# Optimization experiments

Measured on AMD Instinct MI355X. Metric: run time of the kernel, lower is better.

## Reference

```python
import jax, jax.numpy as jnp
import numpy as np

N = 500000
D = 128
R = D // 4  # reduction = 4
G = 2048    # number of graphs


def setup_inputs() -> dict:
    key = jax.random.key(0)
    ks = jax.random.split(key, 8)
    x = jax.random.normal(ks[0], (N, D), dtype=jnp.float32)
    batch = jnp.sort(jax.random.randint(ks[1], (N,), 0, G))
    # SE-gate MLP params (nn.Linear stores weight as [out,in]; we store transposed for x @ W)
    fc_w1 = jax.random.normal(ks[2], (D, R), dtype=jnp.float32) * (1.0 / np.sqrt(D))
    fc_b1 = jnp.zeros((R,), dtype=jnp.float32)
    fc_w2 = jax.random.normal(ks[3], (R, D), dtype=jnp.float32) * (1.0 / np.sqrt(R))
    fc_b2 = jnp.zeros((D,), dtype=jnp.float32)
    # xavier-uniform weight_matrix [D, D]
    lim = np.sqrt(6.0 / (D + D))
    W = jax.random.uniform(ks[4], (D, D), dtype=jnp.float32, minval=-lim, maxval=lim)
    return {"x": x, "batch": batch, "size": G,
            "fc_w1": fc_w1, "fc_b1": fc_b1, "fc_w2": fc_w2, "fc_b2": fc_b2, "W": W}


def reference(x, batch, size, fc_w1, fc_b1, fc_w2, fc_b2, W):
    # gated SE-block: attention = tanh(MLP(x)); x = attention*x + x
    attention = jnp.tanh(jnp.maximum(x @ fc_w1 + fc_b1, 0.0) @ fc_w2 + fc_b2)
    x2 = attention * x + x  # [N, D]
    # global_mean_pool: segment mean over graphs
    seg_sum = jax.ops.segment_sum(x2, batch, num_segments=size)           # [G, D]
    counts = jax.ops.segment_sum(jnp.ones((x2.shape[0],), x2.dtype), batch, num_segments=size)
    mean = seg_sum / jnp.maximum(counts, 1.0)[:, None]                     # [G, D]
    transformed_global = jnp.tanh(mean @ W)                                # [G, D]
    # gather-broadcast per-graph global back to nodes, per-node attention coef
    coefs = jax.nn.sigmoid(jnp.sum(x2 * transformed_global[batch], axis=1))  # [N]
    weighted = coefs[:, None] * x2                                          # [N, D]
    return jax.ops.segment_sum(weighted, batch, num_segments=size)          # [G, D]
```

## Files before the change

kernel.cpp:

```cpp
#include <hip/hip_runtime.h>
#include <hip/hip_bf16.h>

#define DDIM 128
#define RDIM 32
#define PBLK 256
#define BLK  512
#define CAP  160
#define XS2  136
#define HSTR 40

typedef __attribute__((ext_vector_type(8))) short bf16x8;
typedef __attribute__((ext_vector_type(4))) float f32x4;

__device__ __forceinline__ float tanh_fast(float v) {
  float e = __expf(2.f * v);
  return 1.f - 2.f / (e + 1.f);
}
__device__ __forceinline__ float sigmoid_fast(float v) {
  return 1.f / (1.f + __expf(-v));
}
__device__ __forceinline__ unsigned short f2bf(float f) {
  unsigned u = __float_as_uint(f);
  u += 0x7fffu + ((u >> 16) & 1u);
  return (unsigned short)(u >> 16);
}
__device__ __forceinline__ float bf2f(unsigned short s) {
  return __uint_as_float(((unsigned)s) << 16);
}
__device__ __forceinline__ unsigned pkbf(float lo, float hi) {
  __hip_bfloat162 t2 = __float22bfloat162_rn(make_float2(lo, hi));
  return *reinterpret_cast<unsigned*>(&t2);
}
__device__ __forceinline__ int lower_bound(const int* __restrict__ b, int n, int v) {
  int lo = 0, hi = n;
  while (lo < hi) { int m = (lo + hi) >> 1; if (b[m] < v) lo = m + 1; else hi = m; }
  return lo;
}

__global__ void k0_prep(const float* __restrict__ w1, const float* __restrict__ w2,
                        unsigned short* __restrict__ w1tf, unsigned short* __restrict__ w2tf)
{
  const int i  = blockIdx.x * blockDim.x + threadIdx.x;
  const int l  = i & 63;
  const int lr = l & 15, q = l >> 4;
  if (i < 512) {
    const int frag = i >> 6;
    const int mt2 = frag >> 2, kk = frag & 3;
    bf16x8 v;
    #pragma unroll
    for (int j = 0; j < 8; ++j)
      v[j] = (short)f2bf(w1[(size_t)(kk * 32 + q * 8 + j) * RDIM + mt2 * 16 + lr]);
    *(bf16x8*)&w1tf[(size_t)i * 8] = v;
  } else {
    const int mt = (i - 512) >> 6;
    bf16x8 v;
    #pragma unroll
    for (int j = 0; j < 8; ++j)
      v[j] = (short)f2bf(w2[(size_t)(q * 8 + j) * DDIM + mt * 16 + lr]);
    *(bf16x8*)&w2tf[(size_t)(i - 512) * 8] = v;
  }
}

__global__ void kb_bounds(const int* __restrict__ batch, int* __restrict__ bounds,
                          int N, int G)
{
  const int g = blockIdx.x * blockDim.x + threadIdx.x;
  if (g <= G) bounds[g] = lower_bound(batch, N, g);
}

__global__ __launch_bounds__(BLK, 4) void k_fused(
    const float* __restrict__ x,
    const unsigned short* __restrict__ w1tf, const float* __restrict__ b1,
    const unsigned short* __restrict__ w2tf, const float* __restrict__ b2,
    const float* __restrict__ W, const int* __restrict__ bounds,
    float* __restrict__ out, int N)
{
  __shared__ unsigned short w1t[512 * 8];
  __shared__ unsigned short w2t[512 * 8];
  __shared__ unsigned short x2s[CAP * XS2];
  __shared__ unsigned short hs8[8][16 * HSTR];
  __shared__ float part[8][132];
  __shared__ float meanv[DDIM];
  __shared__ float tgs[DDIM];

  const int t  = threadIdx.x;
  const int l  = t & 63;
  const int w  = t >> 6;
  const int lr = l & 15;
  const int q  = l >> 4;
  const int g  = blockIdx.x;
  const int lo = bounds[g], hi = bounds[g + 1];
  const int cnt = hi - lo;
  unsigned short* hs = hs8[w];

  for (int i = t; i < 512; i += BLK) {
    ((bf16x8*)w1t)[i] = ((const bf16x8*)w1tf)[i];
    ((bf16x8*)w2t)[i] = ((const bf16x8*)w2tf)[i];
  }
  __syncthreads();

  auto core = [&](int tb, f32x4 (&cacc)[8]) -> const float* {
    const int ridx = tb + lr;
    const int rcl  = min(ridx, cnt - 1);
    const float* xrow = x + (size_t)(lo + rcl) * DDIM;
    bf16x8 xf[4];
    #pragma unroll
    for (int kk = 0; kk < 4; ++kk) {
      float4 a = *(const float4*)(xrow + kk * 32 + q * 8);
      float4 b = *(const float4*)(xrow + kk * 32 + q * 8 + 4);
      uint4 u;
      u.x = pkbf(a.x, a.y); u.y = pkbf(a.z, a.w);
      u.z = pkbf(b.x, b.y); u.w = pkbf(b.z, b.w);
      xf[kk] = *(bf16x8*)&u;
    }
    f32x4 hacc[2];
    {
      float4 bv0 = *(const float4*)(b1 + q * 4);
      float4 bv1 = *(const float4*)(b1 + 16 + q * 4);
      hacc[0][0] = bv0.x; hacc[0][1] = bv0.y; hacc[0][2] = bv0.z; hacc[0][3] = bv0.w;
      hacc[1][0] = bv1.x; hacc[1][1] = bv1.y; hacc[1][2] = bv1.z; hacc[1][3] = bv1.w;
    }
    #pragma unroll
    for (int kk = 0; kk < 4; ++kk) {
      bf16x8 wa = *(const bf16x8*)&w1t[(size_t)((0 * 4 + kk) * 64 + l) * 8];
      bf16x8 wb = *(const bf16x8*)&w1t[(size_t)((1 * 4 + kk) * 64 + l) * 8];
      hacc[0] = __builtin_amdgcn_mfma_f32_16x16x32_bf16(wa, xf[kk], hacc[0], 0, 0, 0);
      hacc[1] = __builtin_amdgcn_mfma_f32_16x16x32_bf16(wb, xf[kk], hacc[1], 0, 0, 0);
    }
    #pragma unroll
    for (int mt2 = 0; mt2 < 2; ++mt2) {
      float h0 = fmaxf(hacc[mt2][0], 0.f), h1 = fmaxf(hacc[mt2][1], 0.f);
      float h2 = fmaxf(hacc[mt2][2], 0.f), h3 = fmaxf(hacc[mt2][3], 0.f);
      uint2 p; p.x = pkbf(h0, h1); p.y = pkbf(h2, h3);
      *(uint2*)&hs[lr * HSTR + mt2 * 16 + q * 4] = p;
    }
    bf16x8 ah = *(const bf16x8*)&hs[lr * HSTR + q * 8];
    #pragma unroll
    for (int mt = 0; mt < 8; ++mt) {
      float4 bv = *(const float4*)(b2 + mt * 16 + q * 4);
      cacc[mt][0] = bv.x; cacc[mt][1] = bv.y; cacc[mt][2] = bv.z; cacc[mt][3] = bv.w;
    }
    #pragma unroll
    for (int mt = 0; mt < 8; ++mt) {
      bf16x8 wf = *(const bf16x8*)&w2t[(size_t)(mt * 64 + l) * 8];
      cacc[mt] = __builtin_amdgcn_mfma_f32_16x16x32_bf16(wf, ah, cacc[mt], 0, 0, 0);
    }
    return xrow;
  };

  float macc[8][4];
  #pragma unroll
  for (int mt = 0; mt < 8; ++mt)
    #pragma unroll
    for (int c = 0; c < 4; ++c) macc[mt][c] = 0.f;

  const int niter1 = (cnt + 127) >> 7;
  for (int it = 0; it < niter1; ++it) {
    const int tb = it * 128 + w * 16;
    if (tb >= cnt) continue;
    f32x4 cacc[8];
    const float* xrow = core(tb, cacc);
    const int ridx = tb + lr;
    if (ridx < cnt) {
      #pragma unroll
      for (int mt = 0; mt < 8; ++mt) {
        float4 xg = *(const float4*)(xrow + mt * 16 + q * 4);
        float y0 = xg.x * (1.f + tanh_fast(cacc[mt][0]));
        float y1 = xg.y * (1.f + tanh_fast(cacc[mt][1]));
        float y2 = xg.z * (1.f + tanh_fast(cacc[mt][2]));
        float y3 = xg.w * (1.f + tanh_fast(cacc[mt][3]));
        macc[mt][0] += y0; macc[mt][1] += y1;
        macc[mt][2] += y2; macc[mt][3] += y3;
        if (ridx < CAP) {
          uint2 p; p.x = pkbf(y0, y1); p.y = pkbf(y2, y3);
          *(uint2*)&x2s[ridx * XS2 + mt * 16 + q * 4] = p;
        }
      }
    }
  }
  __syncthreads();

  #pragma unroll
  for (int mt = 0; mt < 8; ++mt)
    #pragma unroll
    for (int c = 0; c < 4; ++c) {
      float v = macc[mt][c];
      v += __shfl_xor(v, 1, 64);
      v += __shfl_xor(v, 2, 64);
      v += __shfl_xor(v, 4, 64);
      v += __shfl_xor(v, 8, 64);
      macc[mt][c] = v;
    }
  if (lr == 0) {
    #pragma unroll
    for (int mt = 0; mt < 8; ++mt)
      *(float4*)&part[w][mt * 16 + q * 4] =
          make_float4(macc[mt][0], macc[mt][1], macc[mt][2], macc[mt][3]);
  }
  __syncthreads();
  if (t < DDIM) {
    float m = 0.f;
    #pragma unroll
    for (int w2 = 0; w2 < 8; ++w2) m += part[w2][t];
    meanv[t] = (cnt > 0) ? m / (float)cnt : 0.f;
  }
  __syncthreads();

  {
    const int c = t & 127, s = t >> 7;
    float a = 0.f;
    #pragma unroll
    for (int k = 0; k < 32; ++k)
      a = fmaf(meanv[s * 32 + k], W[(size_t)(s * 32 + k) * DDIM + c], a);
    part[s][c] = a;
  }
  __syncthreads();
  if (t < DDIM)
    tgs[t] = tanh_fast(part[0][t] + part[1][t] + part[2][t] + part[3][t]);
  __syncthreads();

  float oacc[8][4];
  #pragma unroll
  for (int mt = 0; mt < 8; ++mt)
    #pragma unroll
    for (int c = 0; c < 4; ++c) oacc[mt][c] = 0.f;

  const int cap2 = cnt < CAP ? cnt : CAP;
  const int niter2 = (cap2 + 127) >> 7;
  for (int it = 0; it < niter2; ++it) {
    const int tb = it * 128 + w * 16;
    if (tb >= cap2) continue;
    const int ridx = tb + lr;
    const bool v = ridx < cap2;
    const int rr = v ? ridx : 0;
    float xv[8][4];
    float p = 0.f;
    #pragma unroll
    for (int mt = 0; mt < 8; ++mt) {
      uint2 u = *(const uint2*)&x2s[rr * XS2 + mt * 16 + q * 4];
      xv[mt][0] = bf2f((unsigned short)(u.x & 0xffffu));
      xv[mt][1] = bf2f((unsigned short)(u.x >> 16));
      xv[mt][2] = bf2f((unsigned short)(u.y & 0xffffu));
      xv[mt][3] = bf2f((unsigned short)(u.y >> 16));
      float4 tg4 = *(const float4*)&tgs[mt * 16 + q * 4];
      p = fmaf(xv[mt][0], tg4.x, p); p = fmaf(xv[mt][1], tg4.y, p);
      p = fmaf(xv[mt][2], tg4.z, p); p = fmaf(xv[mt][3], tg4.w, p);
    }
    p += __shfl_xor(p, 16, 64);
    p += __shfl_xor(p, 32, 64);
    const float coef = sigmoid_fast(p);
    if (v) {
      #pragma unroll
      for (int mt = 0; mt < 8; ++mt)
        #pragma unroll
        for (int c = 0; c < 4; ++c) oacc[mt][c] = fmaf(coef, xv[mt][c], oacc[mt][c]);
    }
  }

  if (cnt > CAP) {
    const int niter3 = (cnt - CAP + 127) >> 7;
    for (int it = 0; it < niter3; ++it) {
      const int tb = CAP + it * 128 + w * 16;
      if (tb >= cnt) continue;
      f32x4 cacc[8];
      const float* xrow = core(tb, cacc);
      const int ridx = tb + lr;
      const bool v = ridx < cnt;
      float p = 0.f;
      uint2 y2[8];
      #pragma unroll
      for (int mt = 0; mt < 8; ++mt) {
        float4 xg = *(const float4*)(xrow + mt * 16 + q * 4);
        float y0 = xg.x * (1.f + tanh_fast(cacc[mt][0]));
        float y1 = xg.y * (1.f + tanh_fast(cacc[mt][1]));
        float y2v = xg.z * (1.f + tanh_fast(cacc[mt][2]));
        float y3 = xg.w * (1.f + tanh_fast(cacc[mt][3]));
        float4 tg4 = *(const float4*)&tgs[mt * 16 + q * 4];
        p = fmaf(y0, tg4.x, p); p = fmaf(y1, tg4.y, p);
        p = fmaf(y2v, tg4.z, p); p = fmaf(y3, tg4.w, p);
        y2[mt].x = pkbf(y0, y1); y2[mt].y = pkbf(y2v, y3);
      }
      p += __shfl_xor(p, 16, 64);
      p += __shfl_xor(p, 32, 64);
      const float coef = sigmoid_fast(p);
      if (v) {
        #pragma unroll
        for (int mt = 0; mt < 8; ++mt) {
          oacc[mt][0] = fmaf(coef, bf2f((unsigned short)(y2[mt].x & 0xffffu)), oacc[mt][0]);
          oacc[mt][1] = fmaf(coef, bf2f((unsigned short)(y2[mt].x >> 16)),     oacc[mt][1]);
          oacc[mt][2] = fmaf(coef, bf2f((unsigned short)(y2[mt].y & 0xffffu)), oacc[mt][2]);
          oacc[mt][3] = fmaf(coef, bf2f((unsigned short)(y2[mt].y >> 16)),     oacc[mt][3]);
        }
      }
    }
  }
  __syncthreads();

  #pragma unroll
  for (int mt = 0; mt < 8; ++mt)
    #pragma unroll
    for (int c = 0; c < 4; ++c) {
      float v = oacc[mt][c];
      v += __shfl_xor(v, 1, 64);
      v += __shfl_xor(v, 2, 64);
      v += __shfl_xor(v, 4, 64);
      v += __shfl_xor(v, 8, 64);
      oacc[mt][c] = v;
    }
  if (lr == 0) {
    #pragma unroll
    for (int mt = 0; mt < 8; ++mt)
      *(float4*)&part[w][mt * 16 + q * 4] =
          make_float4(oacc[mt][0], oacc[mt][1], oacc[mt][2], oacc[mt][3]);
  }
  __syncthreads();
  if (t < DDIM) {
    float m = 0.f;
    #pragma unroll
    for (int w2 = 0; w2 < 8; ++w2) m += part[w2][t];
    out[(size_t)g * DDIM + t] = m;
  }
}

extern "C" void kernel_launch(void* const* d_in, const int* in_sizes, int n_in,
                              void* d_out, int out_size, void* d_ws, size_t ws_size,
                              hipStream_t stream) {
  const float* x     = (const float*)d_in[0];
  const int*   batch = (const int*)d_in[1];
  const float* w1 = (const float*)d_in[3];
  const float* b1 = (const float*)d_in[4];
  const float* w2 = (const float*)d_in[5];
  const float* b2 = (const float*)d_in[6];
  const float* W  = (const float*)d_in[7];
  float* out = (float*)d_out;

  const int N = in_sizes[0] / DDIM;
  const int G = out_size / DDIM;

  unsigned short* w1tf = (unsigned short*)d_ws;
  unsigned short* w2tf = w1tf + 4096;
  int* bounds = (int*)(w2tf + 4096);
  (void)ws_size; (void)n_in;

  hipLaunchKernelGGL(k0_prep, dim3(4), dim3(PBLK), 0, stream, w1, w2, w1tf, w2tf);
  hipLaunchKernelGGL(kb_bounds, dim3((G + 1 + PBLK - 1) / PBLK), dim3(PBLK), 0, stream,
                     batch, bounds, N, G);
  hipLaunchKernelGGL(k_fused, dim3(G), dim3(BLK), 0, stream,
                     x, w1tf, b1, w2tf, b2, W, bounds, out, N);
}
```

Measured before the change: 156.5 us.

## Halve block size and double-buffer x row loads across iterations

```diff
diff --git a/kernel.cpp b/kernel.cpp
--- a/kernel.cpp
+++ b/kernel.cpp
@@ -4,8 +4,8 @@
 #define DDIM 128
 #define RDIM 32
 #define PBLK 256
-#define BLK  512
-#define CAP  160
+#define BLK  256
+#define CAP  144
 #define XS2  136
 #define HSTR 40
 
@@ -14,10 +14,10 @@
 
 __device__ __forceinline__ float tanh_fast(float v) {
   float e = __expf(2.f * v);
-  return 1.f - 2.f / (e + 1.f);
+  return 1.f - 2.f * __builtin_amdgcn_rcpf(e + 1.f);
 }
 __device__ __forceinline__ float sigmoid_fast(float v) {
-  return 1.f / (1.f + __expf(-v));
+  return __builtin_amdgcn_rcpf(1.f + __expf(-v));
 }
 __device__ __forceinline__ unsigned short f2bf(float f) {
   unsigned u = __float_as_uint(f);
@@ -68,7 +68,7 @@
   if (g <= G) bounds[g] = lower_bound(batch, N, g);
 }
 
-__global__ __launch_bounds__(BLK, 4) void k_fused(
+__global__ __launch_bounds__(BLK, 2) void k_fused(
     const float* __restrict__ x,
     const unsigned short* __restrict__ w1tf, const float* __restrict__ b1,
     const unsigned short* __restrict__ w2tf, const float* __restrict__ b2,
@@ -78,8 +78,8 @@
   __shared__ unsigned short w1t[512 * 8];
   __shared__ unsigned short w2t[512 * 8];
   __shared__ unsigned short x2s[CAP * XS2];
-  __shared__ unsigned short hs8[8][16 * HSTR];
-  __shared__ float part[8][132];
+  __shared__ unsigned short hs4[4][16 * HSTR];
+  __shared__ float part[4][132];
   __shared__ float meanv[DDIM];
   __shared__ float tgs[DDIM];
 
@@ -91,7 +91,7 @@
   const int g  = blockIdx.x;
   const int lo = bounds[g], hi = bounds[g + 1];
   const int cnt = hi - lo;
-  unsigned short* hs = hs8[w];
+  unsigned short* hs = hs4[w];
 
   for (int i = t; i < 512; i += BLK) {
     ((bf16x8*)w1t)[i] = ((const bf16x8*)w1tf)[i];
@@ -99,18 +99,30 @@
   }
   __syncthreads();
 
-  auto core = [&](int tb, f32x4 (&cacc)[8]) -> const float* {
+  auto issue = [&](int tb, float4 (&xfr)[8], float4 (&xg)[8]) {
     const int ridx = tb + lr;
-    const int rcl  = min(ridx, cnt - 1);
+    const int rcl  = (cnt > 0) ? min(ridx, cnt - 1) : 0;
     const float* xrow = x + (size_t)(lo + rcl) * DDIM;
+    #pragma unroll
+    for (int kk = 0; kk < 4; ++kk) {
+      xfr[kk * 2]     = *(const float4*)(xrow + kk * 32 + q * 8);
+      xfr[kk * 2 + 1] = *(const float4*)(xrow + kk * 32 + q * 8 + 4);
+    }
+    #pragma unroll
+    for (int mt = 0; mt < 8; ++mt)
+      xg[mt] = *(const float4*)(xrow + mt * 16 + q * 4);
+  };
+
+  auto compute = [&](const float4 (&xfr)[8], const float4 (&xg)[8],
+                     float (&y)[8][4]) {
     bf16x8 xf[4];
     #pragma unroll
     for (int kk = 0; kk < 4; ++kk) {
-      float4 a = *(const float4*)(xrow + kk * 32 + q * 8);
-      float4 b = *(const float4*)(xrow + kk * 32 + q * 8 + 4);
       uint4 u;
-      u.x = pkbf(a.x, a.y); u.y = pkbf(a.z, a.w);
-      u.z = pkbf(b.x, b.y); u.w = pkbf(b.z, b.w);
+      u.x = pkbf(xfr[kk*2].x,   xfr[kk*2].y);
+      u.y = pkbf(xfr[kk*2].z,   xfr[kk*2].w);
+      u.z = pkbf(xfr[kk*2+1].x, xfr[kk*2+1].y);
+      u.w = pkbf(xfr[kk*2+1].z, xfr[kk*2+1].w);
       xf[kk] = *(bf16x8*)&u;
     }
     f32x4 hacc[2];
@@ -135,6 +147,7 @@
       *(uint2*)&hs[lr * HSTR + mt2 * 16 + q * 4] = p;
     }
     bf16x8 ah = *(const bf16x8*)&hs[lr * HSTR + q * 8];
+    f32x4 cacc[8];
     #pragma unroll
     for (int mt = 0; mt < 8; ++mt) {
       float4 bv = *(const float4*)(b2 + mt * 16 + q * 4);
@@ -145,7 +158,13 @@
       bf16x8 wf = *(const bf16x8*)&w2t[(size_t)(mt * 64 + l) * 8];
       cacc[mt] = __builtin_amdgcn_mfma_f32_16x16x32_bf16(wf, ah, cacc[mt], 0, 0, 0);
     }
-    return xrow;
+    #pragma unroll
+    for (int mt = 0; mt < 8; ++mt) {
+      y[mt][0] = xg[mt].x * (1.f + tanh_fast(cacc[mt][0]));
+      y[mt][1] = xg[mt].y * (1.f + tanh_fast(cacc[mt][1]));
+      y[mt][2] = xg[mt].z * (1.f + tanh_fast(cacc[mt][2]));
+      y[mt][3] = xg[mt].w * (1.f + tanh_fast(cacc[mt][3]));
+    }
   };
 
   float macc[8][4];
@@ -154,27 +173,42 @@
     #pragma unroll
     for (int c = 0; c < 4; ++c) macc[mt][c] = 0.f;
 
-  const int niter1 = (cnt + 127) >> 7;
-  for (int it = 0; it < niter1; ++it) {
-    const int tb = it * 128 + w * 16;
-    if (tb >= cnt) continue;
-    f32x4 cacc[8];
-    const float* xrow = core(tb, cacc);
+  auto p1tail = [&](int tb, float (&y)[8][4]) {
     const int ridx = tb + lr;
     if (ridx < cnt) {
       #pragma unroll
       for (int mt = 0; mt < 8; ++mt) {
-        float4 xg = *(const float4*)(xrow + mt * 16 + q * 4);
-        float y0 = xg.x * (1.f + tanh_fast(cacc[mt][0]));
-        float y1 = xg.y * (1.f + tanh_fast(cacc[mt][1]));
-        float y2 = xg.z * (1.f + tanh_fast(cacc[mt][2]));
-        float y3 = xg.w * (1.f + tanh_fast(cacc[mt][3]));
-        macc[mt][0] += y0; macc[mt][1] += y1;
-        macc[mt][2] += y2; macc[mt][3] += y3;
+        macc[mt][0] += y[mt][0]; macc[mt][1] += y[mt][1];
+        macc[mt][2] += y[mt][2]; macc[mt][3] += y[mt][3];
         if (ridx < CAP) {
-          uint2 p; p.x = pkbf(y0, y1); p.y = pkbf(y2, y3);
+          uint2 p; p.x = pkbf(y[mt][0], y[mt][1]); p.y = pkbf(y[mt][2], y[mt][3]);
           *(uint2*)&x2s[ridx * XS2 + mt * 16 + q * 4] = p;
         }
+      }
+    }
+  };
+
+  {
+    const int niter = (cnt + 63) >> 6;
+    float4 xfA[8], xgA[8], xfB[8], xgB[8];
+    float y[8][4];
+    int it = 0;
+    if (it < niter && it * 64 + w * 16 < cnt) issue(it * 64 + w * 16, xfA, xgA);
+    while (it < niter) {
+      {
+        const int tb = it * 64 + w * 16;
+        const int tn = (it + 1) * 64 + w * 16;
+        if (it + 1 < niter && tn < cnt) issue(tn, xfB, xgB);
+        if (tb < cnt) { compute(xfA, xgA, y); p1tail(tb, y); }
+        ++it;
+      }
+      if (it >= niter) break;
+      {
+        const int tb = it * 64 + w * 16;
+        const int tn = (it + 1) * 64 + w * 16;
+        if (it + 1 < niter && tn < cnt) issue(tn, xfA, xgA);
+        if (tb < cnt) { compute(xfB, xgB, y); p1tail(tb, y); }
+        ++it;
       }
     }
   }
@@ -199,9 +233,7 @@
   }
   __syncthreads();
   if (t < DDIM) {
-    float m = 0.f;
-    #pragma unroll
-    for (int w2 = 0; w2 < 8; ++w2) m += part[w2][t];
+    float m = part[0][t] + part[1][t] + part[2][t] + part[3][t];
     meanv[t] = (cnt > 0) ? m / (float)cnt : 0.f;
   }
   __syncthreads();
@@ -209,14 +241,13 @@
   {
     const int c = t & 127, s = t >> 7;
     float a = 0.f;
-    #pragma unroll
-    for (int k = 0; k < 32; ++k)
-      a = fmaf(meanv[s * 32 + k], W[(size_t)(s * 32 + k) * DDIM + c], a);
+    #pragma unroll 8
+    for (int k = 0; k < 64; ++k)
+      a = fmaf(meanv[s * 64 + k], W[(size_t)(s * 64 + k) * DDIM + c], a);
     part[s][c] = a;
   }
   __syncthreads();
-  if (t < DDIM)
-    tgs[t] = tanh_fast(part[0][t] + part[1][t] + part[2][t] + part[3][t]);
+  if (t < DDIM) tgs[t] = tanh_fast(part[0][t] + part[1][t]);
   __syncthreads();
 
   float oacc[8][4];
@@ -226,9 +257,8 @@
     for (int c = 0; c < 4; ++c) oacc[mt][c] = 0.f;
 
   const int cap2 = cnt < CAP ? cnt : CAP;
-  const int niter2 = (cap2 + 127) >> 7;
-  for (int it = 0; it < niter2; ++it) {
-    const int tb = it * 128 + w * 16;
+  for (int it = 0; it * 64 < cap2; ++it) {
+    const int tb = it * 64 + w * 16;
     if (tb >= cap2) continue;
     const int ridx = tb + lr;
     const bool v = ridx < cap2;
@@ -258,39 +288,51 @@
   }
 
   if (cnt > CAP) {
-    const int niter3 = (cnt - CAP + 127) >> 7;
-    for (int it = 0; it < niter3; ++it) {
-      const int tb = CAP + it * 128 + w * 16;
-      if (tb >= cnt) continue;
-      f32x4 cacc[8];
-      const float* xrow = core(tb, cacc);
+    const int niter = (cnt - CAP + 63) >> 6;
+    float4 xfA[8], xgA[8], xfB[8], xgB[8];
+    float y[8][4];
+    auto p2tail = [&](int tb, float (&yy)[8][4]) {
       const int ridx = tb + lr;
       const bool v = ridx < cnt;
       float p = 0.f;
-      uint2 y2[8];
       #pragma unroll
       for (int mt = 0; mt < 8; ++mt) {
-        float4 xg = *(const float4*)(xrow + mt * 16 + q * 4);
-        float y0 = xg.x * (1.f + tanh_fast(cacc[mt][0]));
-        float y1 = xg.y * (1.f + tanh_fast(cacc[mt][1]));
-        float y2v = xg.z * (1.f + tanh_fast(cacc[mt][2]));
-        float y3 = xg.w * (1.f + tanh_fast(cacc[mt][3]));
         float4 tg4 = *(const float4*)&tgs[mt * 16 + q * 4];
-        p = fmaf(y0, tg4.x, p); p = fmaf(y1, tg4.y, p);
-        p = fmaf(y2v, tg4.z, p); p = fmaf(y3, tg4.w, p);
-        y2[mt].x = pkbf(y0, y1); y2[mt].y = pkbf(y2v, y3);
-      }
+        p = fmaf(yy[mt][0], tg4.x, p); p = fmaf(yy[mt][1], tg4.y, p);
+        p = fmaf(yy[mt][2], tg4.z, p); p = fmaf(yy[mt][3], tg4.w, p);
+      }
+      if (!v) p = 0.f;
       p += __shfl_xor(p, 16, 64);
       p += __shfl_xor(p, 32, 64);
       const float coef = sigmoid_fast(p);
       if (v) {
         #pragma unroll
         for (int mt = 0; mt < 8; ++mt) {
-          oacc[mt][0] = fmaf(coef, bf2f((unsigned short)(y2[mt].x & 0xffffu)), oacc[mt][0]);
-          oacc[mt][1] = fmaf(coef, bf2f((unsigned short)(y2[mt].x >> 16)),     oacc[mt][1]);
-          oacc[mt][2] = fmaf(coef, bf2f((unsigned short)(y2[mt].y & 0xffffu)), oacc[mt][2]);
-          oacc[mt][3] = fmaf(coef, bf2f((unsigned short)(y2[mt].y >> 16)),     oacc[mt][3]);
+          oacc[mt][0] = fmaf(coef, bf2f(f2bf(yy[mt][0])), oacc[mt][0]);
+          oacc[mt][1] = fmaf(coef, bf2f(f2bf(yy[mt][1])), oacc[mt][1]);
+          oacc[mt][2] = fmaf(coef, bf2f(f2bf(yy[mt][2])), oacc[mt][2]);
+          oacc[mt][3] = fmaf(coef, bf2f(f2bf(yy[mt][3])), oacc[mt][3]);
         }
+      }
+    };
+    int it = 0;
+    if (it < niter && CAP + it * 64 + w * 16 < cnt)
+      issue(CAP + it * 64 + w * 16, xfA, xgA);
+    while (it < niter) {
+      {
+        const int tb = CAP + it * 64 + w * 16;
+        const int tn = CAP + (it + 1) * 64 + w * 16;
+        if (it + 1 < niter && tn < cnt) issue(tn, xfB, xgB);
+        if (tb < cnt) { compute(xfA, xgA, y); p2tail(tb, y); }
+        ++it;
+      }
+      if (it >= niter) break;
+      {
+        const int tb = CAP + it * 64 + w * 16;
+        const int tn = CAP + (it + 1) * 64 + w * 16;
+        if (it + 1 < niter && tn < cnt) issue(tn, xfA, xgA);
+        if (tb < cnt) { compute(xfB, xgB, y); p2tail(tb, y); }
+        ++it;
       }
     }
   }
@@ -314,12 +356,8 @@
           make_float4(oacc[mt][0], oacc[mt][1], oacc[mt][2], oacc[mt][3]);
   }
   __syncthreads();
-  if (t < DDIM) {
-    float m = 0.f;
-    #pragma unroll
-    for (int w2 = 0; w2 < 8; ++w2) m += part[w2][t];
-    out[(size_t)g * DDIM + t] = m;
-  }
+  if (t < DDIM)
+    out[(size_t)g * DDIM + t] = part[0][t] + part[1][t] + part[2][t] + part[3][t];
 }
 
 extern "C" void kernel_launch(void* const* d_in, const int* in_sizes, int n_in,
```

Measured after the change: 188.5 us. 1.2x slower.
